# Optimization experiments

Hardware: AMD Instinct MI355X
Metric: run time of the kernel (lower is better)

The kernel has to match this reference:

```python
import jax, jax.numpy as jnp
import numpy as np

MARGIN = 0.3
EPS = 1e-6  # torch TripletMarginLoss pairwise_distance eps


def setup_inputs() -> dict:
    key = jax.random.key(0)
    k1, k2 = jax.random.split(key)
    n, d = 8192, 128
    inputs = jax.random.normal(k1, (n, d), dtype=jnp.float32)
    similarity = jax.random.randint(k2, (n, n), 0, 2, dtype=jnp.int32)
    return {"inputs": inputs, "similarity": similarity}


def reference(inputs, similarity):
    # mask[i, j] = True if j is a positive of anchor i
    mask = similarity != 0                      # (n, n) bool
    maskf = mask.astype(inputs.dtype)
    counts = maskf.sum(axis=1, keepdims=True)   # (n, 1), >0 by construction
    # per-anchor center = mean of its positives (masked mean as a GEMM)
    centers = (maskf @ inputs) / counts         # (n, d)
    # dist[i, j] = ||centers[i] - inputs[j]||_2 via the expansion trick
    # (avoids materializing the (n, n, d) difference tensor of the original)
    c2 = jnp.sum(centers * centers, axis=1)[:, None]
    x2 = jnp.sum(inputs * inputs, axis=1)[None, :]
    d2 = c2 + x2 - 2.0 * (centers @ inputs.T)
    dist = jnp.sqrt(jnp.maximum(d2, 0.0))       # (n, n)
    # dist only feeds argmin in the original (indices carry no grad)
    dist = jax.lax.stop_gradient(dist)
    # hard-negative mining: argmin of dist over negatives of each anchor
    neg_idx = jnp.argmin(jnp.where(mask, jnp.inf, dist), axis=1)  # (n,)
    neg_min = inputs[neg_idx]                   # (n, d)
    # TripletMarginLoss(margin=0.3, p=2): anchor=centers, pos=inputs, neg=neg_min
    d_ap = jnp.linalg.norm(centers - inputs + EPS, axis=1)
    d_an = jnp.linalg.norm(centers - neg_min + EPS, axis=1)
    return jnp.mean(jnp.maximum(d_ap - d_an + MARGIN, 0.0))
```

## Files before the change

kernel.cpp:

```cpp
#include <hip/hip_runtime.h>
#include <stdint.h>

#define NN 8192
#define DD 128

typedef float f32x4 __attribute__((ext_vector_type(4)));
typedef short bf16x8 __attribute__((ext_vector_type(8)));

union B8 { uint32_t u[4]; bf16x8 v; };

__device__ inline uint16_t f2bf(float f) {
  uint32_t u = __builtin_bit_cast(uint32_t, f);
  uint32_t r = (u + 0x7FFFu + ((u >> 16) & 1u)) >> 16;
  return (uint16_t)r;
}

__device__ inline f32x4 mfma16(bf16x8 a, bf16x8 b, f32x4 c) {
  return __builtin_amdgcn_mfma_f32_16x16x32_bf16(a, b, c, 0, 0, 0);
}

__global__ __launch_bounds__(256) void k_prep(const float* __restrict__ inp,
                                              uint16_t* __restrict__ inp_bf,
                                              uint16_t* __restrict__ inpT_bf,
                                              float* __restrict__ x2p) {
  __shared__ uint16_t ldsT[128 * 65];
  __shared__ float ldsS[256];
  const int tid = threadIdx.x;
  const int j0 = blockIdx.x * 64;
  const int r = tid >> 2;
  const int dseg = (tid & 3) * 32;
  float ss = 0.f;
#pragma unroll
  for (int it = 0; it < 8; ++it) {
    float4 v = *(const float4*)(inp + (size_t)(j0 + r) * DD + dseg + it * 4);
    ss += v.x * v.x + v.y * v.y + v.z * v.z + v.w * v.w;
    uint16_t b0 = f2bf(v.x), b1 = f2bf(v.y), b2 = f2bf(v.z), b3 = f2bf(v.w);
    *(ushort4*)(inp_bf + (size_t)(j0 + r) * DD + dseg + it * 4) = make_ushort4(b0, b1, b2, b3);
    int d = dseg + it * 4;
    ldsT[(d + 0) * 65 + r] = b0;
    ldsT[(d + 1) * 65 + r] = b1;
    ldsT[(d + 2) * 65 + r] = b2;
    ldsT[(d + 3) * 65 + r] = b3;
  }
  ldsS[tid] = ss;
  __syncthreads();
  if (tid < 64)
    x2p[j0 + tid] = ldsS[tid * 4] + ldsS[tid * 4 + 1] + ldsS[tid * 4 + 2] + ldsS[tid * 4 + 3] + 512.0f;
#pragma unroll
  for (int it = 0; it < 32; ++it) {
    int flat = it * 256 + tid;
    int d = flat >> 6, jl = flat & 63;
    inpT_bf[(size_t)d * NN + j0 + jl] = ldsT[d * 65 + jl];
  }
}

__global__ __launch_bounds__(256) void k_bitgen(const int* __restrict__ sim,
                                                uint32_t* __restrict__ bmT,
                                                uint32_t* __restrict__ counts) {
  __shared__ uint32_t ldsW[64 * 64];
  const int tid = threadIdx.x, lane = tid & 63, w = tid >> 6;
  const int m0 = blockIdx.x * 64;
  const int c0 = blockIdx.y * 2048;
#pragma unroll 1
  for (int rr = 0; rr < 16; ++rr) {
    const int rl = rr * 4 + w;
    const int row = m0 + rl;
    const int* p = sim + (size_t)row * NN + c0 + lane;
    int v[32];
#pragma unroll
    for (int s = 0; s < 32; ++s) v[s] = p[s * 64];
    uint32_t cnt = 0;
#pragma unroll
    for (int s = 0; s < 32; ++s) {
      unsigned long long ball = __ballot(v[s] != 0);
      cnt += (uint32_t)__popcll(ball);
      if ((lane & 31) == 0)
        ldsW[(s * 2 + (lane >> 5)) * 64 + rl] = (uint32_t)(ball >> (lane & 32));
    }
    if (lane == 0) atomicAdd(&counts[row], cnt);
  }
  __syncthreads();
#pragma unroll
  for (int it = 0; it < 16; ++it) {
    int idx = it * 256 + tid;
    int kw = idx >> 6, r = idx & 63;
    bmT[(size_t)((c0 >> 5) + kw) * NN + m0 + r] = ldsW[idx];
  }
}

__global__ __launch_bounds__(256, 4) void k_gemm1(const uint16_t* __restrict__ inpT,
                                                  const uint32_t* __restrict__ bmT,
                                                  float* __restrict__ part) {
  __shared__ __align__(16) uint16_t ldsB[128 * 40];
  __shared__ uint32_t ldsM[64];
  const int tid = threadIdx.x, lane = tid & 63, w = tid >> 6;
  const int col = lane & 15, quad = lane >> 4;
  const int m0 = blockIdx.x * 64;
  const int kb0 = blockIdx.y * 1024;
  const int wm = (w >> 1) * 32, wn = (w & 1) * 64;
  const int dim = tid >> 1, koff = (tid & 1) * 16;
  f32x4 acc[2][4];
  const f32x4 z = {0.f, 0.f, 0.f, 0.f};
#pragma unroll
  for (int r = 0; r < 2; ++r)
#pragma unroll
    for (int c = 0; c < 4; ++c) acc[r][c] = z;

  bf16x8 bpf0 = *(const bf16x8*)(inpT + (size_t)dim * NN + kb0 + koff);
  bf16x8 bpf1 = *(const bf16x8*)(inpT + (size_t)dim * NN + kb0 + koff + 8);
  uint32_t mpf = (tid < 64) ? bmT[(size_t)(kb0 >> 5) * NN + m0 + tid] : 0u;

  for (int ks = 0; ks < 32; ++ks) {
    const int kb = kb0 + ks * 32;
    __syncthreads();
    *(bf16x8*)(ldsB + dim * 40 + koff) = bpf0;
    *(bf16x8*)(ldsB + dim * 40 + koff + 8) = bpf1;
    if (tid < 64) ldsM[tid] = mpf;
    __syncthreads();
    if (ks < 31) {
      bpf0 = *(const bf16x8*)(inpT + (size_t)dim * NN + kb + 32 + koff);
      bpf1 = *(const bf16x8*)(inpT + (size_t)dim * NN + kb + 32 + koff + 8);
      if (tid < 64) mpf = bmT[(size_t)((kb + 32) >> 5) * NN + m0 + tid];
    }
    B8 af[2];
#pragma unroll
    for (int rr = 0; rr < 2; ++rr) {
      uint32_t word = ldsM[wm + rr * 16 + col];
      uint32_t b = (word >> (quad * 8)) & 0xFFu;
      uint32_t s = b * 0x8001u;
#pragma unroll
      for (int p = 0; p < 4; ++p) {
        uint32_t t = (s >> (2 * p)) & 0x10001u;
        af[rr].u[p] = t * 0x3F80u;
      }
    }
#pragma unroll
    for (int cc = 0; cc < 4; ++cc) {
      bf16x8 bfr = *(const bf16x8*)(ldsB + (wn + cc * 16 + col) * 40 + quad * 8);
#pragma unroll
      for (int rr = 0; rr < 2; ++rr) acc[rr][cc] = mfma16(af[rr].v, bfr, acc[rr][cc]);
    }
  }
  float* pp = part + (size_t)blockIdx.y * NN * DD;
#pragma unroll
  for (int rr = 0; rr < 2; ++rr)
#pragma unroll
    for (int cc = 0; cc < 4; ++cc)
#pragma unroll
      for (int g = 0; g < 4; ++g)
        pp[(size_t)(m0 + wm + rr * 16 + quad * 4 + g) * DD + wn + cc * 16 + col] = acc[rr][cc][g];
}

__global__ __launch_bounds__(256) void k_reduce(const float* __restrict__ part,
                                                const uint32_t* __restrict__ counts,
                                                float* __restrict__ centers,
                                                uint16_t* __restrict__ cen_bf) {
  const int gid = blockIdx.x * 256 + threadIdx.x;
  const int idx = gid * 4;
  const int row = idx >> 7;
  const float inv = 1.0f / (float)counts[row];
  float4 v = *(const float4*)(part + idx);
#pragma unroll
  for (int s = 1; s < 8; ++s) {
    float4 u = *(const float4*)(part + (size_t)s * NN * DD + idx);
    v.x += u.x; v.y += u.y; v.z += u.z; v.w += u.w;
  }
  v.x *= inv; v.y *= inv; v.z *= inv; v.w *= inv;
  *(float4*)(centers + idx) = v;
  *(ushort4*)(cen_bf + idx) = make_ushort4(f2bf(v.x), f2bf(v.y), f2bf(v.z), f2bf(v.w));
}

__global__ __launch_bounds__(256, 4) void k_argmin(const uint16_t* __restrict__ cen_bf,
                                                   const uint16_t* __restrict__ inp_bf,
                                                   const uint32_t* __restrict__ bmT,
                                                   const float* __restrict__ x2p,
                                                   uint32_t* __restrict__ negkey) {
  __shared__ __align__(16) uint16_t ldsB[64 * 136];
  __shared__ uint32_t ldsM[128];
  __shared__ float ldsX[64];
  __shared__ uint32_t ldsR[64];
  const int tid = threadIdx.x, lane = tid & 63, w = tid >> 6;
  const int col = lane & 15, quad = lane >> 4;
  const int i0 = blockIdx.x * 64;
  const int jbase = blockIdx.y * 1024;
  const int wi = (w >> 1) * 32, wj = (w & 1) * 32;
  bf16x8 af[2][4];
#pragma unroll
  for (int rr = 0; rr < 2; ++rr)
#pragma unroll
    for (int kk = 0; kk < 4; ++kk)
      af[rr][kk] = *(const bf16x8*)(cen_bf + (size_t)(i0 + wi + rr * 16 + col) * DD + kk * 32 + quad * 8);
  if (tid < 64) ldsR[tid] = 0xFFFFFFFFu;
  uint32_t best[2][4];
#pragma unroll
  for (int rr = 0; rr < 2; ++rr)
#pragma unroll
    for (int g = 0; g < 4; ++g) best[rr][g] = 0xFFFFFFFFu;

  const int jl = tid >> 2, doff = (tid & 3) * 32;
  bf16x8 bpf[4];
#pragma unroll
  for (int it = 0; it < 4; ++it)
    bpf[it] = *(const bf16x8*)(inp_bf + (size_t)(jbase + jl) * DD + doff + it * 8);
  uint32_t mpf = (tid < 128) ? bmT[(size_t)((jbase >> 5) + (tid >> 6)) * NN + i0 + (tid & 63)] : 0u;
  float xpf = (tid >= 128 && tid < 192) ? x2p[jbase + tid - 128] : 0.f;

  for (int js = 0; js < 16; ++js) {
    const int j0 = jbase + js * 64;
    __syncthreads();
#pragma unroll
    for (int it = 0; it < 4; ++it)
      *(bf16x8*)(ldsB + jl * 136 + doff + it * 8) = bpf[it];
    if (tid < 128) ldsM[tid] = mpf;
    else if (tid < 192) ldsX[tid - 128] = xpf;
    __syncthreads();
    if (js < 15) {
#pragma unroll
      for (int it = 0; it < 4; ++it)
        bpf[it] = *(const bf16x8*)(inp_bf + (size_t)(j0 + 64 + jl) * DD + doff + it * 8);
      if (tid < 128) mpf = bmT[(size_t)(((j0 + 64) >> 5) + (tid >> 6)) * NN + i0 + (tid & 63)];
      else if (tid < 192) xpf = x2p[j0 + 64 + tid - 128];
    }
    f32x4 acc[2][2];
    const f32x4 z = {0.f, 0.f, 0.f, 0.f};
    acc[0][0] = z; acc[0][1] = z; acc[1][0] = z; acc[1][1] = z;
#pragma unroll
    for (int kk = 0; kk < 4; ++kk) {
      bf16x8 b0 = *(const bf16x8*)(ldsB + (wj + col) * 136 + kk * 32 + quad * 8);
      bf16x8 b1 = *(const bf16x8*)(ldsB + (wj + 16 + col) * 136 + kk * 32 + quad * 8);
      acc[0][0] = mfma16(af[0][kk], b0, acc[0][0]);
      acc[0][1] = mfma16(af[0][kk], b1, acc[0][1]);
      acc[1][0] = mfma16(af[1][kk], b0, acc[1][0]);
      acc[1][1] = mfma16(af[1][kk], b1, acc[1][1]);
    }
    const uint32_t wsel = (w & 1) * 64;
    uint32_t words[2][4];
#pragma unroll
    for (int rr = 0; rr < 2; ++rr)
#pragma unroll
      for (int g = 0; g < 4; ++g) words[rr][g] = ldsM[wsel + wi + rr * 16 + quad * 4 + g];
#pragma unroll
    for (int cc = 0; cc < 2; ++cc) {
      const int jj = wj + cc * 16 + col;
      const float xq = ldsX[jj];
      const uint32_t jpre = (uint32_t)(j0 + jj);
      const int sh = 31 - (cc * 16 + col);
#pragma unroll
      for (int rr = 0; rr < 2; ++rr)
#pragma unroll
        for (int g = 0; g < 4; ++g) {
          float v = fmaf(-2.0f, acc[rr][cc][g], xq);
          uint32_t u = __builtin_bit_cast(uint32_t, v);
          uint32_t key = (u & 0xFFFFE000u) | jpre;
          key |= (words[rr][g] << sh) & 0x80000000u;
          best[rr][g] = min(best[rr][g], key);
        }
    }
  }
#pragma unroll
  for (int rr = 0; rr < 2; ++rr)
#pragma unroll
    for (int g = 0; g < 4; ++g) {
      uint32_t k = best[rr][g];
#pragma unroll
      for (int d = 1; d < 16; d <<= 1) {
        uint32_t o = (uint32_t)__shfl_xor((int)k, d);
        k = min(k, o);
      }
      if (col == 0) atomicMin(&ldsR[wi + rr * 16 + quad * 4 + g], k);
    }
  __syncthreads();
  if (tid < 64) atomicMin(&negkey[i0 + tid], ldsR[tid]);
}

__global__ __launch_bounds__(256) void k_loss(const float* __restrict__ centers,
                                              const float* __restrict__ inp,
                                              const uint32_t* __restrict__ negkey,
                                              float* __restrict__ out) {
  __shared__ float lds[4];
  const int tid = threadIdx.x, lane = tid & 63, w = tid >> 6;
  float local = 0.f;
#pragma unroll 1
  for (int a = 0; a < 4; ++a) {
    int i = blockIdx.x * 16 + w * 4 + a;
    float2 c = *(const float2*)(centers + (size_t)i * DD + lane * 2);
    float2 x = *(const float2*)(inp + (size_t)i * DD + lane * 2);
    uint32_t ni = negkey[i] & (NN - 1);
    float2 gv = *(const float2*)(inp + (size_t)ni * DD + lane * 2);
    float e0 = c.x - x.x + 1e-6f, e1 = c.y - x.y + 1e-6f;
    float f0 = c.x - gv.x + 1e-6f, f1 = c.y - gv.y + 1e-6f;
    float dap = e0 * e0 + e1 * e1;
    float dan = f0 * f0 + f1 * f1;
#pragma unroll
    for (int d = 32; d; d >>= 1) {
      dap += __shfl_down(dap, d);
      dan += __shfl_down(dan, d);
    }
    if (lane == 0) local += fmaxf(sqrtf(dap) - sqrtf(dan) + 0.3f, 0.f);
  }
  if (lane == 0) lds[w] = local;
  __syncthreads();
  if (tid == 0) atomicAdd(out, (lds[0] + lds[1] + lds[2] + lds[3]) * (1.0f / 8192.0f));
}

extern "C" void kernel_launch(void* const* d_in, const int* in_sizes, int n_in,
                              void* d_out, int out_size, void* d_ws, size_t ws_size,
                              hipStream_t stream) {
  (void)in_sizes; (void)n_in; (void)ws_size;
  const float* inp = (const float*)d_in[0];
  const int* sim = (const int*)d_in[1];
  float* out = (float*)d_out;
  char* ws = (char*)d_ws;

  uint32_t* bmT     = (uint32_t*)ws;
  float* part       = (float*)(ws + (8u << 20));
  float* centers    = (float*)(ws + (40u << 20));
  uint16_t* inp_bf  = (uint16_t*)(ws + (44u << 20));
  uint16_t* inpT_bf = (uint16_t*)(ws + (46u << 20));
  uint16_t* cen_bf  = (uint16_t*)(ws + (48u << 20));
  float* x2p        = (float*)(ws + (50u << 20));
  uint32_t* counts  = (uint32_t*)(ws + (50u << 20) + 32768u);
  uint32_t* negkey  = (uint32_t*)(ws + (50u << 20) + 65536u);

  hipMemsetAsync(counts, 0, NN * sizeof(uint32_t), stream);
  hipMemsetAsync(negkey, 0xFF, NN * sizeof(uint32_t), stream);
  hipMemsetAsync(out, 0, out_size * sizeof(float), stream);

  k_prep<<<128, 256, 0, stream>>>(inp, inp_bf, inpT_bf, x2p);
  k_bitgen<<<dim3(128, 4), 256, 0, stream>>>(sim, bmT, counts);
  k_gemm1<<<dim3(128, 8), 256, 0, stream>>>(inpT_bf, bmT, part);
  k_reduce<<<1024, 256, 0, stream>>>(part, counts, centers, cen_bf);
  k_argmin<<<dim3(128, 8), 256, 0, stream>>>(cen_bf, inp_bf, bmT, x2p, negkey);
  k_loss<<<512, 256, 0, stream>>>(centers, inp, negkey, out);
}
```

Baseline: 451.6 us.

## Fold memsets into prep, double-buffer bitgen loads, widen gemm1 K-step

Replaces the three hipMemsetAsync calls with initialisation inside k_prep, removing separate launches. k_bitgen now prefetches the next row's similarity values into a second register buffer while processing the current row, which hides global load latency at the cost of more registers (launch bounds set to 2 blocks). k_gemm1 stages 64 k-elements per iteration instead of 32, halving the number of barrier pairs per tile. This uses more LDS and registers per block.

```diff
diff --git a/kernel.cpp b/kernel.cpp
--- a/kernel.cpp
+++ b/kernel.cpp
@@ -22,10 +22,16 @@
 __global__ __launch_bounds__(256) void k_prep(const float* __restrict__ inp,
                                               uint16_t* __restrict__ inp_bf,
                                               uint16_t* __restrict__ inpT_bf,
-                                              float* __restrict__ x2p) {
+                                              float* __restrict__ x2p,
+                                              uint32_t* __restrict__ counts,
+                                              uint32_t* __restrict__ negkey,
+                                              float* __restrict__ out) {
   __shared__ uint16_t ldsT[128 * 65];
   __shared__ float ldsS[256];
   const int tid = threadIdx.x;
+  const int gid = blockIdx.x * 256 + tid;
+  if (gid < NN) { counts[gid] = 0u; negkey[gid] = 0xFFFFFFFFu; }
+  if (gid == 0) out[0] = 0.f;
   const int j0 = blockIdx.x * 64;
   const int r = tid >> 2;
   const int dseg = (tid & 3) * 32;
@@ -54,30 +60,38 @@
   }
 }
 
-__global__ __launch_bounds__(256) void k_bitgen(const int* __restrict__ sim,
-                                                uint32_t* __restrict__ bmT,
-                                                uint32_t* __restrict__ counts) {
+__global__ __launch_bounds__(256, 2) void k_bitgen(const int* __restrict__ sim,
+                                                   uint32_t* __restrict__ bmT,
+                                                   uint32_t* __restrict__ counts) {
   __shared__ uint32_t ldsW[64 * 64];
   const int tid = threadIdx.x, lane = tid & 63, w = tid >> 6;
   const int m0 = blockIdx.x * 64;
   const int c0 = blockIdx.y * 2048;
+  int va[32], vb[32];
+  {
+    const int* p = sim + (size_t)(m0 + w) * NN + c0 + lane;
+#pragma unroll
+    for (int s = 0; s < 32; ++s) va[s] = p[s * 64];
+  }
 #pragma unroll 1
   for (int rr = 0; rr < 16; ++rr) {
     const int rl = rr * 4 + w;
-    const int row = m0 + rl;
-    const int* p = sim + (size_t)row * NN + c0 + lane;
-    int v[32];
-#pragma unroll
-    for (int s = 0; s < 32; ++s) v[s] = p[s * 64];
+    if (rr < 15) {
+      const int* p = sim + (size_t)(m0 + rl + 4) * NN + c0 + lane;
+#pragma unroll
+      for (int s = 0; s < 32; ++s) vb[s] = p[s * 64];
+    }
     uint32_t cnt = 0;
 #pragma unroll
     for (int s = 0; s < 32; ++s) {
-      unsigned long long ball = __ballot(v[s] != 0);
+      unsigned long long ball = __ballot(va[s] != 0);
       cnt += (uint32_t)__popcll(ball);
       if ((lane & 31) == 0)
         ldsW[(s * 2 + (lane >> 5)) * 64 + rl] = (uint32_t)(ball >> (lane & 32));
     }
-    if (lane == 0) atomicAdd(&counts[row], cnt);
+    if (lane == 0) atomicAdd(&counts[m0 + rl], cnt);
+#pragma unroll
+    for (int s = 0; s < 32; ++s) va[s] = vb[s];
   }
   __syncthreads();
 #pragma unroll
@@ -91,14 +105,15 @@
 __global__ __launch_bounds__(256, 4) void k_gemm1(const uint16_t* __restrict__ inpT,
                                                   const uint32_t* __restrict__ bmT,
                                                   float* __restrict__ part) {
-  __shared__ __align__(16) uint16_t ldsB[128 * 40];
-  __shared__ uint32_t ldsM[64];
+  __shared__ __align__(16) uint16_t ldsB[128 * 72];
+  __shared__ uint32_t ldsM[128];
   const int tid = threadIdx.x, lane = tid & 63, w = tid >> 6;
   const int col = lane & 15, quad = lane >> 4;
   const int m0 = blockIdx.x * 64;
   const int kb0 = blockIdx.y * 1024;
   const int wm = (w >> 1) * 32, wn = (w & 1) * 64;
-  const int dim = tid >> 1, koff = (tid & 1) * 16;
+  const int dim = tid >> 1, koff = (tid & 1) * 32;
+  const int mrow = tid >> 1, msel = tid & 1;
   f32x4 acc[2][4];
   const f32x4 z = {0.f, 0.f, 0.f, 0.f};
 #pragma unroll
@@ -106,39 +121,46 @@
 #pragma unroll
     for (int c = 0; c < 4; ++c) acc[r][c] = z;
 
-  bf16x8 bpf0 = *(const bf16x8*)(inpT + (size_t)dim * NN + kb0 + koff);
-  bf16x8 bpf1 = *(const bf16x8*)(inpT + (size_t)dim * NN + kb0 + koff + 8);
-  uint32_t mpf = (tid < 64) ? bmT[(size_t)(kb0 >> 5) * NN + m0 + tid] : 0u;
-
-  for (int ks = 0; ks < 32; ++ks) {
-    const int kb = kb0 + ks * 32;
+  bf16x8 bpf[4];
+#pragma unroll
+  for (int it = 0; it < 4; ++it)
+    bpf[it] = *(const bf16x8*)(inpT + (size_t)dim * NN + kb0 + koff + it * 8);
+  uint32_t mpf = (tid < 128) ? bmT[(size_t)((kb0 >> 5) + msel) * NN + m0 + mrow] : 0u;
+
+  for (int ks = 0; ks < 16; ++ks) {
+    const int kb = kb0 + ks * 64;
     __syncthreads();
-    *(bf16x8*)(ldsB + dim * 40 + koff) = bpf0;
-    *(bf16x8*)(ldsB + dim * 40 + koff + 8) = bpf1;
-    if (tid < 64) ldsM[tid] = mpf;
+#pragma unroll
+    for (int it = 0; it < 4; ++it)
+      *(bf16x8*)(ldsB + dim * 72 + koff + it * 8) = bpf[it];
+    if (tid < 128) ldsM[mrow * 2 + msel] = mpf;
     __syncthreads();
-    if (ks < 31) {
-      bpf0 = *(const bf16x8*)(inpT + (size_t)dim * NN + kb + 32 + koff);
-      bpf1 = *(const bf16x8*)(inpT + (size_t)dim * NN + kb + 32 + koff + 8);
-      if (tid < 64) mpf = bmT[(size_t)((kb + 32) >> 5) * NN + m0 + tid];
-    }
-    B8 af[2];
-#pragma unroll
-    for (int rr = 0; rr < 2; ++rr) {
-      uint32_t word = ldsM[wm + rr * 16 + col];
-      uint32_t b = (word >> (quad * 8)) & 0xFFu;
-      uint32_t s = b * 0x8001u;
-#pragma unroll
-      for (int p = 0; p < 4; ++p) {
-        uint32_t t = (s >> (2 * p)) & 0x10001u;
-        af[rr].u[p] = t * 0x3F80u;
+    if (ks < 15) {
+#pragma unroll
+      for (int it = 0; it < 4; ++it)
+        bpf[it] = *(const bf16x8*)(inpT + (size_t)dim * NN + kb + 64 + koff + it * 8);
+      if (tid < 128) mpf = bmT[(size_t)(((kb + 64) >> 5) + msel) * NN + m0 + mrow];
+    }
+#pragma unroll
+    for (int h = 0; h < 2; ++h) {
+      B8 af[2];
+#pragma unroll
+      for (int rr = 0; rr < 2; ++rr) {
+        uint32_t word = ldsM[(wm + rr * 16 + col) * 2 + h];
+        uint32_t b = (word >> (quad * 8)) & 0xFFu;
+        uint32_t s = b * 0x8001u;
+#pragma unroll
+        for (int p = 0; p < 4; ++p) {
+          uint32_t t = (s >> (2 * p)) & 0x10001u;
+          af[rr].u[p] = t * 0x3F80u;
+        }
       }
-    }
-#pragma unroll
-    for (int cc = 0; cc < 4; ++cc) {
-      bf16x8 bfr = *(const bf16x8*)(ldsB + (wn + cc * 16 + col) * 40 + quad * 8);
-#pragma unroll
-      for (int rr = 0; rr < 2; ++rr) acc[rr][cc] = mfma16(af[rr].v, bfr, acc[rr][cc]);
+#pragma unroll
+      for (int cc = 0; cc < 4; ++cc) {
+        bf16x8 bfr = *(const bf16x8*)(ldsB + (wn + cc * 16 + col) * 72 + h * 32 + quad * 8);
+#pragma unroll
+        for (int rr = 0; rr < 2; ++rr) acc[rr][cc] = mfma16(af[rr].v, bfr, acc[rr][cc]);
+      }
     }
   }
   float* pp = part + (size_t)blockIdx.y * NN * DD;
@@ -306,7 +328,7 @@
 extern "C" void kernel_launch(void* const* d_in, const int* in_sizes, int n_in,
                               void* d_out, int out_size, void* d_ws, size_t ws_size,
                               hipStream_t stream) {
-  (void)in_sizes; (void)n_in; (void)ws_size;
+  (void)in_sizes; (void)n_in; (void)out_size; (void)ws_size;
   const float* inp = (const float*)d_in[0];
   const int* sim = (const int*)d_in[1];
   float* out = (float*)d_out;
@@ -322,11 +344,7 @@
   uint32_t* counts  = (uint32_t*)(ws + (50u << 20) + 32768u);
   uint32_t* negkey  = (uint32_t*)(ws + (50u << 20) + 65536u);
 
-  hipMemsetAsync(counts, 0, NN * sizeof(uint32_t), stream);
-  hipMemsetAsync(negkey, 0xFF, NN * sizeof(uint32_t), stream);
-  hipMemsetAsync(out, 0, out_size * sizeof(float), stream);
-
-  k_prep<<<128, 256, 0, stream>>>(inp, inp_bf, inpT_bf, x2p);
+  k_prep<<<128, 256, 0, stream>>>(inp, inp_bf, inpT_bf, x2p, counts, negkey, out);
   k_bitgen<<<dim3(128, 4), 256, 0, stream>>>(sim, bmT, counts);
   k_gemm1<<<dim3(128, 8), 256, 0, stream>>>(inpT_bf, bmT, part);
   k_reduce<<<1024, 256, 0, stream>>>(part, counts, centers, cen_bf);
```

New measurement: 446.7 us, median of 2. No clear change (-1.1%).
